# Optimization experiments

Measured on AMD Instinct MI355X. Metric: run time of the kernel, lower is better.

The kernel has to match this reference:

```python
import jax, jax.numpy as jnp
from jax import lax
import numpy as np

D_MODEL = 1024
D_STATE = 64
D_CONV = 4
EXPAND = 2
HEADDIM = 64
D_INNER = EXPAND * D_MODEL          # 2048
NHEADS = D_INNER // HEADDIM         # 32
CHUNK = 64
CONV_DIM = D_INNER + 2 * D_STATE    # 2176
D_IN_PROJ = 2 * D_INNER + 2 * D_STATE + NHEADS  # 4256
B_SZ = 4
SEQLEN = 2048
EPS = 1e-5


def _silu(x):
    return x * jax.nn.sigmoid(x)


def _segsum(x):
    # x: [..., T]; returns [..., T, T] with [i,j] = sum_{j<k<=i} x[k], -inf above diag
    T = x.shape[-1]
    xe = jnp.broadcast_to(x[..., None], x.shape + (T,))
    strict_lower = jnp.tril(jnp.ones((T, T), bool), -1)
    xe = jnp.where(strict_lower, xe, 0.0)
    s = jnp.cumsum(xe, axis=-2)
    lower = jnp.tril(jnp.ones((T, T), bool), 0)
    return jnp.where(lower, s, -jnp.inf)


def setup_inputs() -> dict:
    key = jax.random.key(0)
    ks = jax.random.split(key, 5)
    u = jax.random.normal(ks[0], (B_SZ, SEQLEN, D_MODEL), jnp.float32)
    W_in = jax.random.normal(ks[1], (D_IN_PROJ, D_MODEL), jnp.float32) * 0.02
    conv_w = jax.random.normal(ks[2], (CONV_DIM, 1, D_CONV), jnp.float32) * 0.2  # depthwise kernel
    conv_b = jnp.zeros((CONV_DIM,), jnp.float32)
    dt_bias = jax.random.uniform(ks[3], (NHEADS,), jnp.float32, -1.0, 1.0)
    A_log = jnp.log(jnp.linspace(1.0, float(NHEADS), NHEADS)).astype(jnp.float32)
    D = jnp.ones((NHEADS,), jnp.float32)
    norm_w = jnp.ones((D_INNER,), jnp.float32)
    W_out = jax.random.normal(ks[4], (D_MODEL, D_INNER), jnp.float32) * 0.02
    return dict(u=u, W_in=W_in, conv_w=conv_w, conv_b=conv_b, dt_bias=dt_bias,
                A_log=A_log, D=D, norm_w=norm_w, W_out=W_out)


def reference(u, W_in, conv_w, conv_b, dt_bias, A_log, D, norm_w, W_out):
    b, s, _ = u.shape
    A = -jnp.exp(A_log)                                   # [H]
    zxbcdt = u @ W_in.T                                   # [b,s,D_IN_PROJ]
    z = zxbcdt[..., :D_INNER]
    xBC = zxbcdt[..., D_INNER:D_INNER + CONV_DIM]
    dt = jax.nn.softplus(zxbcdt[..., D_INNER + CONV_DIM:] + dt_bias)  # [b,s,H]

    # causal depthwise conv1d (left pad d_conv-1 == torch pad-both + slice[:s])
    xc = lax.conv_general_dilated(
        xBC.transpose(0, 2, 1), conv_w, window_strides=(1,),
        padding=[(D_CONV - 1, 0)], feature_group_count=CONV_DIM,
        dimension_numbers=('NCH', 'OIH', 'NCH'))
    xBC = _silu(xc.transpose(0, 2, 1) + conv_b)           # [b,s,CONV_DIM]

    x = xBC[..., :D_INNER].reshape(b, s, NHEADS, HEADDIM)
    Bm = xBC[..., D_INNER:D_INNER + D_STATE]              # [b,s,N]
    Cm = xBC[..., D_INNER + D_STATE:]                     # [b,s,N]

    # SSD chunked scan
    nch = s // CHUNK
    xs = (x * dt[..., None]).reshape(b, nch, CHUNK, NHEADS, HEADDIM)
    Ad = (A * dt).reshape(b, nch, CHUNK, NHEADS)
    Br = Bm.reshape(b, nch, CHUNK, D_STATE)
    Cr = Cm.reshape(b, nch, CHUNK, D_STATE)
    A_ch = Ad.transpose(0, 1, 3, 2)                       # [b,c,h,l]
    A_cum = jnp.cumsum(A_ch, axis=-1)
    L = jnp.exp(_segsum(A_ch))                            # [b,c,h,l,l]
    Y_diag = jnp.einsum('bcln,bcsn,bchls,bcshp->bclhp', Cr, Br, L, xs)
    decay_states = jnp.exp(A_cum[..., -1:] - A_cum)       # [b,c,h,l]
    states = jnp.einsum('bchl,bcln,bclhp->bchpn', decay_states, Br, xs)
    init = jnp.zeros((b, 1, NHEADS, HEADDIM, D_STATE), xs.dtype)
    states = jnp.concatenate([init, states], axis=1)      # [b,c+1,h,p,n]
    total_decay = jnp.pad(A_cum[..., -1].transpose(0, 2, 1), ((0, 0), (0, 0), (1, 0)))
    decay_chunk = jnp.exp(_segsum(total_decay))           # [b,h,c+1,c+1]
    new_states = jnp.einsum('bhzc,bchpn->bzhpn', decay_chunk, states)
    states = new_states[:, :-1]                           # [b,c,h,p,n]
    state_decay_out = jnp.exp(A_cum)
    Y_off = jnp.einsum('bcln,bchpn,bchl->bclhp', Cr, states, state_decay_out)
    y = (Y_diag + Y_off).reshape(b, s, NHEADS, HEADDIM)

    y = y + x * D[:, None]
    y = y.reshape(b, s, D_INNER)
    # gated RMSNorm
    y = y * _silu(z)
    y = y * lax.rsqrt(jnp.mean(y * y, axis=-1, keepdims=True) + EPS) * norm_w
    return y @ W_out.T
```

## Files before the change

kernel.cpp:

```cpp
#include <hip/hip_runtime.h>
#include <hip/hip_bf16.h>

#define BSZ 4
#define SEQ 2048
#define DMODEL 1024
#define DINNER 2048
#define DSTATE 64
#define NH 32
#define HD 64
#define CKL 64
#define NCH 32
#define CONVD 2176
#define DPROJ 4256
#define N1 4224
#define MTOT 8192
#define YSTR 72
#define YSTR2 120
#define CVTB 6272

typedef __hip_bfloat16 bf16;
typedef __attribute__((ext_vector_type(8))) short short8;
typedef __attribute__((ext_vector_type(4))) short short4_;
typedef __attribute__((ext_vector_type(4))) float f32x4;

__device__ __forceinline__ float sigmoidf_(float x) { return 1.0f / (1.0f + __expf(-x)); }
__device__ __forceinline__ float bits2f(short s) { return __uint_as_float(((unsigned)(unsigned short)s) << 16); }
__device__ __forceinline__ short f2bits(float f) {
    bf16 h = __float2bfloat16(f);
    return *reinterpret_cast<short*>(&h);
}

__device__ __forceinline__ void gl_lds16(const bf16* g, bf16* l) {
    __builtin_amdgcn_global_load_lds((const __attribute__((address_space(1))) void*)g,
                                     (__attribute__((address_space(3))) void*)l, 16, 0, 0);
}

__device__ __forceinline__ f32x4 MF(short8 a, short8 b, f32x4 c) {
    return __builtin_amdgcn_mfma_f32_16x16x32_bf16(a, b, c, 0, 0, 0);
}

template<int N> __device__ __forceinline__ void vmw() {
    if constexpr (N == 0)      asm volatile("s_waitcnt vmcnt(0)" ::: "memory");
    else if constexpr (N == 3) asm volatile("s_waitcnt vmcnt(3)" ::: "memory");
    else if constexpr (N == 6) asm volatile("s_waitcnt vmcnt(6)" ::: "memory");
    else                       asm volatile("s_waitcnt vmcnt(15)" ::: "memory");
}

__device__ __forceinline__ void swzx(int& bx, int& by) {
    int nx = gridDim.x;
    int nwg = nx * gridDim.y;
    int Lr = blockIdx.y * nx + blockIdx.x;
    int L = (Lr & 7) * (nwg >> 3) + (Lr >> 3);
    int GSZ = nx * 8;
    int g = L / GSZ, r = L - g * GSZ;
    bx = r % nx;
    by = g * 8 + r / nx;
}

__global__ __launch_bounds__(256) void k_pre2(const float* __restrict__ u, const float* __restrict__ W_in,
                                              const float* __restrict__ dt_bias,
                                              const float* __restrict__ W_out, const float* __restrict__ nw,
                                              bf16* __restrict__ u_b, float* __restrict__ dtt,
                                              bf16* __restrict__ win_b, bf16* __restrict__ wout_b) {
    __shared__ __align__(16) float us[8 * DMODEL];
    const int tid = threadIdx.x;
    if (blockIdx.x < CVTB) {
        int g = (blockIdx.x * 256 + tid) * 4;
        if (g < N1 * DMODEL) {
            f32x4 f = *(const f32x4*)&W_in[g];
            short4_ o;
#pragma unroll
            for (int j = 0; j < 4; j++) o[j] = f2bits(f[j]);
            *(short4_*)&win_b[g] = o;
        } else if (g < N1 * DMODEL + DMODEL * DINNER) {
            int g2 = g - N1 * DMODEL;
            f32x4 f = *(const f32x4*)&W_out[g2];
            f32x4 w = *(const f32x4*)&nw[g2 & (DINNER - 1)];
            short4_ o;
#pragma unroll
            for (int j = 0; j < 4; j++) o[j] = f2bits(f[j] * w[j]);
            *(short4_*)&wout_b[g2] = o;
        }
        return;
    }
    const int t0 = (blockIdx.x - CVTB) * 8;
    const float* ur = u + (size_t)t0 * DMODEL;
    bf16* ub = u_b + (size_t)t0 * DMODEL;
#pragma unroll
    for (int i = 0; i < 8; i++) {
        int idx = (i * 256 + tid) * 4;
        f32x4 v = *(const f32x4*)&ur[idx];
        *(f32x4*)&us[idx] = v;
        short4_ o;
#pragma unroll
        for (int j = 0; j < 4; j++) o[j] = f2bits(v[j]);
        *(short4_*)&ub[idx] = o;
    }
    __syncthreads();
    const int h = tid >> 3, sub = tid & 7;
    const float* wr = W_in + (size_t)(DPROJ - NH + h) * DMODEL;
    float s[8] = {};
    for (int k = sub * 4; k < DMODEL; k += 32) {
        f32x4 w4 = *(const f32x4*)&wr[k];
#pragma unroll
        for (int rr = 0; rr < 8; rr++) {
            f32x4 u4 = *(const f32x4*)&us[rr * DMODEL + k];
            s[rr] += u4[0] * w4[0] + u4[1] * w4[1] + u4[2] * w4[2] + u4[3] * w4[3];
        }
    }
#pragma unroll
    for (int rr = 0; rr < 8; rr++) {
        s[rr] += __shfl_down(s[rr], 4, 8);
        s[rr] += __shfl_down(s[rr], 2, 8);
        s[rr] += __shfl_down(s[rr], 1, 8);
    }
    if (sub == 0) {
        float bh = dt_bias[h];
#pragma unroll
        for (int rr = 0; rr < 8; rr++) {
            float x = s[rr] + bh;
            dtt[(size_t)h * MTOT + t0 + rr] = (x > 20.f) ? x : log1pf(__expf(x));
        }
    }
}

__global__ __launch_bounds__(256) void k_dts(const float* __restrict__ dtt, const float* __restrict__ A_log,
                                             float* __restrict__ sAc, float* __restrict__ sfv,
                                             float* __restrict__ etot) {
    const int h = blockIdx.x, b = blockIdx.y;
    const int tid = threadIdx.x, w = tid >> 6, lane = tid & 63;
    const float Ah = -__expf(A_log[h]);
#pragma unroll
    for (int g = 0; g < 8; g++) {
        int c = g * 4 + w;
        int t0 = b * SEQ + c * CKL;
        float dv = dtt[(size_t)h * MTOT + t0 + lane];
        float v = Ah * dv;
#pragma unroll
        for (int d = 1; d < 64; d <<= 1) { float o = __shfl_up(v, d); if (lane >= d) v += o; }
        float tot = __shfl(v, 63);
        sAc[(size_t)h * MTOT + t0 + lane] = v;
        sfv[(size_t)h * MTOT + t0 + lane] = __expf(tot - v) * dv;
        if (lane == 63) etot[(h * BSZ + b) * NCH + c] = __expf(tot);
    }
}

#define BARWAIT()                                           \
    __builtin_amdgcn_s_barrier();                           \
    asm volatile("s_waitcnt lgkmcnt(0)" ::: "memory");      \
    __builtin_amdgcn_sched_barrier(0);                      \
    __builtin_amdgcn_s_setprio(1)
#define ENDPH()                                             \
    __builtin_amdgcn_s_setprio(0);                          \
    __builtin_amdgcn_s_barrier()

__global__ __launch_bounds__(512, 2) void k_g1(const bf16* __restrict__ Ap,
                                               const bf16* __restrict__ Wp,
                                               bf16* __restrict__ Cp) {
    __shared__ __align__(16) short sA[2][16384];
    __shared__ __align__(16) short sB[2][12288];
    const int tid = threadIdx.x;
    const int lane = tid & 63, w = tid >> 6;
    const int wm = w >> 2, wn = w & 3;
    const int lr = lane & 15, lk = lane >> 4;
    int bx, by; swzx(bx, by);
    const int m0 = by * 256, n0 = bx * 192;
    const int ld = DMODEL;

    const int r8 = tid >> 3;
    const int c8 = ((tid & 7) ^ (r8 & 7)) * 8;
    const bf16* pA = Ap + (size_t)(m0 + r8) * ld + c8;
    const bf16* pB = Wp + (size_t)(n0 + r8) * ld + c8;

    auto stA = [&](int d, int t) {
#pragma unroll
        for (int h = 0; h < 2; h++)
#pragma unroll
            for (int q = 0; q < 2; q++)
                gl_lds16(pA + (size_t)(h * 128 + q * 64) * ld + t * 64,
                         (bf16*)&sA[d][h * 8192 + q * 4096 + tid * 8]);
    };
    auto stB = [&](int d, int u, int t) {
        gl_lds16(pB + (size_t)(u * 64) * ld + t * 64,
                 (bf16*)&sB[d][u * 4096 + tid * 8]);
    };

    const int c0 = (lk ^ (lr & 7)) * 8;
    const int c1 = ((lk + 4) ^ (lr & 7)) * 8;
    const int aR = (wm * 128 + lr) * 64;
    const int bR = (wn * 48 + lr) * 64;

    f32x4 acc[8][3];
#pragma unroll
    for (int i = 0; i < 8; i++)
#pragma unroll
        for (int j = 0; j < 3; j++) acc[i][j] = (f32x4){0.f, 0.f, 0.f, 0.f};
    short8 bfr[3][2], af[2][2];

#define RDA1(D, I)                                                   \
    af[0][0] = *(const short8*)&sA[D][aR + (I) * 1024 + c0];         \
    af[0][1] = *(const short8*)&sA[D][aR + (I) * 1024 + c1];         \
    af[1][0] = *(const short8*)&sA[D][aR + (I + 1) * 1024 + c0];     \
    af[1][1] = *(const short8*)&sA[D][aR + (I + 1) * 1024 + c1]
#define RDB1(D)                                                      \
    _Pragma("unroll")                                                \
    for (int jn = 0; jn < 3; ++jn) {                                 \
        bfr[jn][0] = *(const short8*)&sB[D][bR + jn * 1024 + c0];    \
        bfr[jn][1] = *(const short8*)&sB[D][bR + jn * 1024 + c1];    \
    }
#define MM1(I)                                                       \
    _Pragma("unroll")                                                \
    for (int hh = 0; hh < 2; ++hh) {                                 \
        _Pragma("unroll")                                            \
        for (int jn = 0; jn < 3; ++jn) {                             \
            acc[I][jn]     = MF(af[0][hh], bfr[jn][hh], acc[I][jn]); \
            acc[I + 1][jn] = MF(af[1][hh], bfr[jn][hh], acc[I + 1][jn]); \
        }                                                            \
    }

    stB(0, 0, 0); stB(0, 1, 0); stB(0, 2, 0); stA(0, 0);
    stB(1, 0, 1); stB(1, 1, 1); stB(1, 2, 1);
    vmw<3>();
    __builtin_amdgcn_s_barrier();

    for (int t0 = 0; t0 < 16; t0 += 2) {
        const int t1 = t0 + 1, t2 = t0 + 2, t3 = t0 + 3;
        const bool more = (t2 < 16);
        RDB1(0); RDA1(0, 0);
        stA(1, t1);
        BARWAIT(); MM1(0); ENDPH();
        RDA1(0, 2); if (more) stB(0, 0, t2);
        BARWAIT(); MM1(2); ENDPH();
        RDA1(0, 4); if (more) stB(0, 1, t2);
        BARWAIT(); MM1(4); ENDPH();
        RDA1(0, 6); if (more) stB(0, 2, t2);
        BARWAIT(); MM1(6);
        __builtin_amdgcn_s_setprio(0);
        if (more) vmw<3>(); else vmw<0>();
        __builtin_amdgcn_s_barrier();
        RDB1(1); RDA1(1, 0);
        if (more) stA(0, t2);
        BARWAIT(); MM1(0); ENDPH();
        RDA1(1, 2); if (more) stB(1, 0, t3);
        BARWAIT(); MM1(2); ENDPH();
        RDA1(1, 4); if (more) stB(1, 1, t3);
        BARWAIT(); MM1(4); ENDPH();
        RDA1(1, 6); if (more) stB(1, 2, t3);
        BARWAIT(); MM1(6);
        __builtin_amdgcn_s_setprio(0);
        if (more) vmw<3>();
        __builtin_amdgcn_s_barrier();
    }
#undef RDA1
#undef RDB1
#undef MM1

#pragma unroll
    for (int im = 0; im < 8; im++) {
        int row = m0 + wm * 128 + im * 16 + lk * 4;
#pragma unroll
        for (int jn = 0; jn < 3; jn++) {
            int col = n0 + wn * 48 + jn * 16 + lr;
            bf16* cp = Cp + (size_t)row * N1 + col;
#pragma unroll
            for (int rr = 0; rr < 4; rr++) cp[(size_t)rr * N1] = __float2bfloat16(acc[im][jn][rr]);
        }
    }
}

__global__ __launch_bounds__(512, 2) void k_g2(const bf16* __restrict__ Ap,
                                               const bf16* __restrict__ Wp,
                                               float* __restrict__ Cp) {
    __shared__ __align__(16) short sA[3][16384];
    __shared__ __align__(16) short sB[3][8192];
    __shared__ float rsrow[256];
    const int tid = threadIdx.x;
    const int lane = tid & 63, w = tid >> 6;
    const int wm = w >> 1, wn = w & 1;
    const int lr = lane & 15, lk = lane >> 4;
    int bx, by; swzx(bx, by);
    const int m0 = by * 256, n0 = bx * 128;
    const int lda = N1, ldb = DINNER;

    const int r8 = tid >> 3;
    const int c8 = ((tid & 7) ^ (r8 & 7)) * 8;
    const bf16* pA = Ap + (size_t)(m0 + r8) * lda + c8;
    const bf16* pB = Wp + (size_t)(n0 + r8) * ldb + c8;

    auto stA = [&](int d, int t) {
#pragma unroll
        for (int h = 0; h < 2; h++)
#pragma unroll
            for (int q = 0; q < 2; q++)
                gl_lds16(pA + (size_t)(h * 128 + q * 64) * lda + t * 64,
                         (bf16*)&sA[d][h * 8192 + q * 4096 + tid * 8]);
    };
    auto stB = [&](int d, int t) {
#pragma unroll
        for (int q = 0; q < 2; q++)
            gl_lds16(pB + (size_t)(q * 64) * ldb + t * 64,
                     (bf16*)&sB[d][q * 4096 + tid * 8]);
    };

    const int c0 = (lk ^ (lr & 7)) * 8;
    const int c1 = ((lk + 4) ^ (lr & 7)) * 8;
    const int aR = (wm * 64 + lr) * 64;
    const int bR = (wn * 64 + lr) * 64;

    f32x4 acc[4][4];
#pragma unroll
    for (int i = 0; i < 4; i++)
#pragma unroll
        for (int j = 0; j < 4; j++) acc[i][j] = (f32x4){0.f, 0.f, 0.f, 0.f};
    float ssq[4] = {0.f, 0.f, 0.f, 0.f};
    short8 bfr[4][2], af[2][2];

#define RDA2(D, I)                                                   \
    af[0][0] = *(const short8*)&sA[D][aR + (I) * 1024 + c0];         \
    af[0][1] = *(const short8*)&sA[D][aR + (I) * 1024 + c1];         \
    af[1][0] = *(const short8*)&sA[D][aR + (I + 1) * 1024 + c0];     \
    af[1][1] = *(const short8*)&sA[D][aR + (I + 1) * 1024 + c1]
#define RDB2(D)                                                      \
    _Pragma("unroll")                                                \
    for (int jn = 0; jn < 4; ++jn) {                                 \
        bfr[jn][0] = *(const short8*)&sB[D][bR + jn * 1024 + c0];    \
        bfr[jn][1] = *(const short8*)&sB[D][bR + jn * 1024 + c1];    \
    }
#define MM2(I)                                                       \
    _Pragma("unroll")                                                \
    for (int hh = 0; hh < 2; ++hh) {                                 \
        _Pragma("unroll")                                            \
        for (int jn = 0; jn < 4; ++jn) {                             \
            acc[I][jn]     = MF(af[0][hh], bfr[jn][hh], acc[I][jn]); \
            acc[I + 1][jn] = MF(af[1][hh], bfr[jn][hh], acc[I + 1][jn]); \
        }                                                            \
    }
#define SSQ2(I)                                                      \
    _Pragma("unroll")                                                \
    for (int hh = 0; hh < 2; ++hh)                                   \
        _Pragma("unroll")                                            \
        for (int e = 0; e < 8; ++e) {                                \
            float v0 = bits2f(af[0][hh][e]), v1 = bits2f(af[1][hh][e]); \
            ssq[I] += v0 * v0; ssq[I + 1] += v1 * v1;                \
        }

    stB(0, 0); stA(0, 0);
    stB(1, 1); stA(1, 1);
    vmw<6>();
    __builtin_amdgcn_s_barrier();

    int rb = 0, sb = 2;
    for (int t = 0; t < 32; ++t) {
        const bool more = (t + 2 < 32);
        RDB2(rb); RDA2(rb, 0);
        if (more) stB(sb, t + 2);
        BARWAIT(); MM2(0); SSQ2(0); ENDPH();
        RDA2(rb, 2);
        if (more) stA(sb, t + 2);
        BARWAIT(); MM2(2); SSQ2(2);
        __builtin_amdgcn_s_setprio(0);
        if (more) vmw<6>(); else if (t + 1 < 32) vmw<0>();
        __builtin_amdgcn_s_barrier();
        rb = (rb == 2) ? 0 : rb + 1;
        sb = (sb == 2) ? 0 : sb + 1;
    }
#undef RDA2
#undef RDB2
#undef MM2
#undef SSQ2

#pragma unroll
    for (int im = 0; im < 4; im++) {
        float s = ssq[im];
        s += __shfl_down(s, 32);
        s += __shfl_down(s, 16);
        if (lane < 16) rsrow[wm * 64 + im * 16 + lane] = rsqrtf(s * (1.0f / DINNER) + 1e-5f);
    }
    __syncthreads();
#pragma unroll
    for (int im = 0; im < 4; im++) {
        int rl = wm * 64 + im * 16 + lk * 4;
        int row = m0 + rl;
#pragma unroll
        for (int rr = 0; rr < 4; rr++) {
            float s = rsrow[rl + rr];
#pragma unroll
            for (int jn = 0; jn < 4; jn++) {
                int col = n0 + wn * 64 + jn * 16 + lr;
                Cp[(size_t)(row + rr) * DMODEL + col] = acc[im][jn][rr] * s;
            }
        }
    }
}

__global__ __launch_bounds__(256) void k_conv(const bf16* __restrict__ zx, const float* __restrict__ cw,
                                              const float* __restrict__ cb, bf16* __restrict__ xbc) {
    const int g = blockIdx.x * 256 + threadIdx.x;
    const int c0 = (g % 544) * 4;
    const int t0 = (g / 544) * 4;
    const int s0 = t0 & (SEQ - 1);
    const short* base = (const short*)(zx + (size_t)t0 * N1 + DINNER + c0);
    f32x4 w0 = *(const f32x4*)&cw[(c0 + 0) * 4];
    f32x4 w1 = *(const f32x4*)&cw[(c0 + 1) * 4];
    f32x4 w2 = *(const f32x4*)&cw[(c0 + 2) * 4];
    f32x4 w3 = *(const f32x4*)&cw[(c0 + 3) * 4];
    f32x4 bias = *(const f32x4*)&cb[c0];
    short4_ v[7];
#pragma unroll
    for (int o = 0; o < 7; o++) {
        if (s0 + o - 3 >= 0) v[o] = *(const short4_*)(base + (long)(o - 3) * N1);
        else v[o] = (short4_){0, 0, 0, 0};
    }
#pragma unroll
    for (int j = 0; j < 4; j++) {
        f32x4 a = bias;
#pragma unroll
        for (int k = 0; k < 4; k++) {
            short4_ x = v[j + k];
            a[0] += bits2f(x[0]) * w0[k];
            a[1] += bits2f(x[1]) * w1[k];
            a[2] += bits2f(x[2]) * w2[k];
            a[3] += bits2f(x[3]) * w3[k];
        }
        short4_ o_;
#pragma unroll
        for (int jj = 0; jj < 4; jj++) o_[jj] = f2bits(a[jj] * sigmoidf_(a[jj]));
        *(short4_*)((short*)xbc + (size_t)(t0 + j) * CONVD + c0) = o_;
    }
}

__global__ __launch_bounds__(512) void k_ssd(const bf16* __restrict__ xbc, const float* __restrict__ dtt,
                                             const float* __restrict__ sAc, const float* __restrict__ sfv,
                                             const float* __restrict__ etg, const float* __restrict__ Dp,
                                             bf16* __restrict__ zx) {
    __shared__ __align__(16) short Ct[2][64 * YSTR];
    __shared__ __align__(16) short Bt[2][64 * YSTR];
    __shared__ __align__(16) short Bn[2][64 * YSTR2];
    __shared__ __align__(16) short Xt[2][32 * YSTR2];
    __shared__ __align__(16) short Sb[2][32 * YSTR];
    __shared__ __align__(16) short Gs[4 * 16 * YSTR];
    __shared__ __align__(16) float Sf[32 * 68];
    __shared__ __align__(16) float sdt2[2][64], sAc2[2][64];
    __shared__ float etl[NCH];

    const int ph = blockIdx.x, h = blockIdx.y, b = blockIdx.z;
    const int tid = threadIdx.x;
    const bool prod = tid >= 256;
    const int ct = tid & 255;
    const int lane = ct & 63, w = ct >> 6;
    const int lr = lane & 15, lk = lane >> 4;
    const float Dh = Dp[h];
    const int xcol = h * HD + ph * 32;

    const int lrow = ct >> 2, c0 = (ct & 3) * 16, px = (ct & 3) * 8;
    const int zl = 16 * w + (lane >> 2), zp = (lane & 3) * 8;

    short8 rC0, rC1, rB0, rB1, rX;
    float rdt, rsa, rsf;
    auto load_chunk = [&](int cc) {
        int rows0 = b * SEQ + cc * CKL;
        const short* rp = (const short*)(xbc + (size_t)(rows0 + lrow) * CONVD);
        rC0 = *(const short8*)&rp[DINNER + DSTATE + c0];
        rC1 = *(const short8*)&rp[DINNER + DSTATE + c0 + 8];
        rB0 = *(const short8*)&rp[DINNER + c0];
        rB1 = *(const short8*)&rp[DINNER + c0 + 8];
        rX  = *(const short8*)&rp[xcol + px];
        rdt = dtt[(size_t)h * MTOT + rows0 + (ct & 63)];
        rsa = sAc[(size_t)h * MTOT + rows0 + (ct & 63)];
        rsf = sfv[(size_t)h * MTOT + rows0 + lrow];
    };
    auto scatter = [&](int buf) {
        *(short8*)&Ct[buf][lrow * YSTR + c0] = rC0;
        *(short8*)&Ct[buf][lrow * YSTR + c0 + 8] = rC1;
        *(short8*)&Bt[buf][lrow * YSTR + c0] = rB0;
        *(short8*)&Bt[buf][lrow * YSTR + c0 + 8] = rB1;
#pragma unroll
        for (int j = 0; j < 8; j++) {
            int n0_ = c0 + j, n1_ = c0 + 8 + j, p_ = px + j;
            Bn[buf][n0_ * YSTR2 + lrow + (n0_ >> 3) * 8] = f2bits(bits2f(rB0[j]) * rsf);
            Bn[buf][n1_ * YSTR2 + lrow + (n1_ >> 3) * 8] = f2bits(bits2f(rB1[j]) * rsf);
            Xt[buf][p_ * YSTR2 + lrow + (p_ >> 3) * 8] = rX[j];
        }
        if (ct < 64) { sdt2[buf][ct] = rdt; sAc2[buf][ct] = rsa; }
    };

    for (int i = tid; i < 32 * 68; i += 512) Sf[i] = 0.f;
    for (int i = tid; i < 32 * YSTR; i += 512) Sb[0][i] = 0;
    if (tid < NCH) etl[tid] = etg[(h * BSZ + b) * NCH + tid];
    if (prod) { load_chunk(0); scatter(0); }
    __syncthreads();

    for (int c = 0; c < NCH; c++) {
        const int par = c & 1, nb = par ^ 1;
        const int rows0 = b * SEQ + c * CKL;
        if (prod) {
            if (c + 1 < NCH) { load_chunk(c + 1); scatter(nb); }
        } else {
            float etot = etl[c];
            short8 zcur = *(const short8*)((const short*)zx + (size_t)(rows0 + zl) * N1 + xcol + zp);

            short8 cf0 = *(const short8*)&Ct[par][(16 * w + lr) * YSTR + lk * 8];
            short8 cf1 = *(const short8*)&Ct[par][(16 * w + lr) * YSTR + 32 + lk * 8];
            f32x4 acc[2];
#pragma unroll
            for (int t = 0; t < 2; t++) {
                short8 s0 = *(const short8*)&Sb[par][(16 * t + lr) * YSTR + lk * 8];
                short8 s1 = *(const short8*)&Sb[par][(16 * t + lr) * YSTR + 32 + lk * 8];
                acc[t] = MF(cf0, s0, (f32x4){0.f, 0.f, 0.f, 0.f});
                acc[t] = MF(cf1, s1, acc[t]);
            }
            float sAcl[4], el[4];
#pragma unroll
            for (int rr = 0; rr < 4; rr++) { sAcl[rr] = sAc2[par][16 * w + lk * 4 + rr]; el[rr] = __expf(sAcl[rr]); }
#pragma unroll
            for (int t = 0; t < 2; t++)
#pragma unroll
                for (int rr = 0; rr < 4; rr++) acc[t][rr] *= el[rr];
            short* gw = Gs + w * 16 * YSTR;
#pragma unroll
            for (int t = 0; t < 4; t++) {
                short8 b0 = *(const short8*)&Bt[par][(16 * t + lr) * YSTR + lk * 8];
                short8 b1 = *(const short8*)&Bt[par][(16 * t + lr) * YSTR + 32 + lk * 8];
                f32x4 g = MF(cf0, b0, (f32x4){0.f, 0.f, 0.f, 0.f});
                g = MF(cf1, b1, g);
                int s = 16 * t + lr;
                float sAcs = sAc2[par][s], dts = sdt2[par][s];
#pragma unroll
                for (int rr = 0; rr < 4; rr++) {
                    int l = 16 * w + lk * 4 + rr;
                    float v = (s <= l) ? g[rr] * __expf(sAcl[rr] - sAcs) * dts : 0.f;
                    gw[(lk * 4 + rr) * YSTR + s] = f2bits(v);
                }
            }
            short8 gf0 = *(const short8*)&gw[lr * YSTR + lk * 8];
            short8 gf1 = *(const short8*)&gw[lr * YSTR + 32 + lk * 8];
#pragma unroll
            for (int t = 0; t < 2; t++) {
                int xr = 16 * t + lr;
                short8 x0 = *(const short8*)&Xt[par][xr * YSTR2 + ((xr >> 3) + lk) * 8];
                short8 x1 = *(const short8*)&Xt[par][xr * YSTR2 + 32 + ((xr >> 3) + lk) * 8];
                acc[t] = MF(gf0, x0, acc[t]);
                acc[t] = MF(gf1, x1, acc[t]);
            }
            {
                int pw = w & 1, nh2 = w >> 1;
                const int xp = 16 * pw + lr;
                short8 xt0 = *(const short8*)&Xt[par][xp * YSTR2 + ((xp >> 3) + lk) * 8];
                short8 xt1 = *(const short8*)&Xt[par][xp * YSTR2 + 32 + ((xp >> 3) + lk) * 8];
#pragma unroll
                for (int j = 0; j < 2; j++) {
                    int nt = 2 * nh2 + j;
                    int nr = 16 * nt + lr;
                    short8 b0 = *(const short8*)&Bn[par][nr * YSTR2 + ((nr >> 3) + lk) * 8];
                    short8 b1 = *(const short8*)&Bn[par][nr * YSTR2 + 32 + ((nr >> 3) + lk) * 8];
                    f32x4 sacc = MF(xt0, b0, (f32x4){0.f, 0.f, 0.f, 0.f});
                    sacc = MF(xt1, b1, sacc);
#pragma unroll
                    for (int rr = 0; rr < 4; rr++) {
                        int n = 16 * nt + lr;
                        int p = 16 * pw + lk * 4 + rr;
                        float nv = Sf[p * 68 + n] * etot + sacc[rr];
                        Sf[p * 68 + n] = nv;
                        Sb[nb][p * YSTR + n] = f2bits(nv);
                    }
                }
            }
#pragma unroll
            for (int t = 0; t < 2; t++) {
#pragma unroll
                for (int rr = 0; rr < 4; rr++) {
                    int p = 16 * t + lr;
                    int l = 16 * w + lk * 4 + rr;
                    float y = acc[t][rr] + Dh * bits2f(Xt[par][p * YSTR2 + l + (p >> 3) * 8]);
                    Ct[par][l * YSTR + p] = f2bits(y);
                }
            }
            {
                short8 y8 = *(const short8*)&Ct[par][zl * YSTR + zp];
                short* zpp = (short*)zx + (size_t)(rows0 + zl) * N1 + xcol + zp;
                short8 o;
#pragma unroll
                for (int j = 0; j < 8; j++) {
                    float z = bits2f(zcur[j]);
                    o[j] = f2bits(bits2f(y8[j]) * (z * sigmoidf_(z)));
                }
                *(short8*)zpp = o;
            }
        }
        __syncthreads();
    }
}

extern "C" void kernel_launch(void* const* d_in, const int* in_sizes, int n_in,
                              void* d_out, int out_size, void* d_ws, size_t ws_size,
                              hipStream_t stream) {
    const float* u       = (const float*)d_in[0];
    const float* W_in    = (const float*)d_in[1];
    const float* conv_w  = (const float*)d_in[2];
    const float* conv_b  = (const float*)d_in[3];
    const float* dt_bias = (const float*)d_in[4];
    const float* A_log   = (const float*)d_in[5];
    const float* Dp      = (const float*)d_in[6];
    const float* norm_w  = (const float*)d_in[7];
    const float* W_out   = (const float*)d_in[8];
    float* out = (float*)d_out;

    char* ws = (char*)d_ws;
    bf16* zx     = (bf16*)ws;  ws += (size_t)MTOT * N1 * 2;
    bf16* xbc    = (bf16*)ws;  ws += (size_t)MTOT * CONVD * 2;
    bf16* wout_b = (bf16*)ws;  ws += (size_t)DMODEL * DINNER * 2;
    float* dtt   = (float*)ws; ws += (size_t)NH * MTOT * 4;
    float* sAcw  = (float*)ws; ws += (size_t)NH * MTOT * 4;
    float* sfvw  = (float*)ws; ws += (size_t)NH * MTOT * 4;
    float* etotw = (float*)ws; ws += 64 * 1024;

    bf16* u_b   = (bf16*)d_out;
    bf16* win_b = (bf16*)((char*)d_out + (size_t)MTOT * DMODEL * 2);

    k_pre2<<<CVTB + MTOT / 8, 256, 0, stream>>>(u, W_in, dt_bias, W_out, norm_w,
                                                u_b, dtt, win_b, wout_b);
    k_dts<<<dim3(NH, BSZ), 256, 0, stream>>>(dtt, A_log, sAcw, sfvw, etotw);

    k_g1<<<dim3(N1 / 192, MTOT / 256), 512, 0, stream>>>(u_b, win_b, zx);

    k_conv<<<(MTOT / 4) * (CONVD / 4) / 256, 256, 0, stream>>>(zx, conv_w, conv_b, xbc);

    k_ssd<<<dim3(2, NH, BSZ), 512, 0, stream>>>(xbc, dtt, sAcw, sfvw, etotw, Dp, zx);

    k_g2<<<dim3(DMODEL / 128, MTOT / 256), 512, 0, stream>>>(zx, wout_b, out);
}
```

Measured before the change: 350.5 us.

## Fuse causal depthwise conv and SiLU into the SSD producer loads

Removes the standalone conv kernel and its intermediate xBC buffer. The SSD kernel's producer threads now read the raw projection output with a 4-row causal window and apply the depthwise conv, bias and SiLU in registers before scattering into shared memory. This is meant to avoid a full write and re-read of the conv activation tensor and one kernel launch. In exchange, the B/C conv is recomputed by every head block, and the producer path carries more loads and math per chunk, which could stall the consumer warps. The same pointer is now passed as both the read-only input and the written output, so correctness depends on which columns the kernel writes.

```diff
diff --git a/kernel.cpp b/kernel.cpp
--- a/kernel.cpp
+++ b/kernel.cpp
@@ -393,45 +393,10 @@
     }
 }
 
-__global__ __launch_bounds__(256) void k_conv(const bf16* __restrict__ zx, const float* __restrict__ cw,
-                                              const float* __restrict__ cb, bf16* __restrict__ xbc) {
-    const int g = blockIdx.x * 256 + threadIdx.x;
-    const int c0 = (g % 544) * 4;
-    const int t0 = (g / 544) * 4;
-    const int s0 = t0 & (SEQ - 1);
-    const short* base = (const short*)(zx + (size_t)t0 * N1 + DINNER + c0);
-    f32x4 w0 = *(const f32x4*)&cw[(c0 + 0) * 4];
-    f32x4 w1 = *(const f32x4*)&cw[(c0 + 1) * 4];
-    f32x4 w2 = *(const f32x4*)&cw[(c0 + 2) * 4];
-    f32x4 w3 = *(const f32x4*)&cw[(c0 + 3) * 4];
-    f32x4 bias = *(const f32x4*)&cb[c0];
-    short4_ v[7];
-#pragma unroll
-    for (int o = 0; o < 7; o++) {
-        if (s0 + o - 3 >= 0) v[o] = *(const short4_*)(base + (long)(o - 3) * N1);
-        else v[o] = (short4_){0, 0, 0, 0};
-    }
-#pragma unroll
-    for (int j = 0; j < 4; j++) {
-        f32x4 a = bias;
-#pragma unroll
-        for (int k = 0; k < 4; k++) {
-            short4_ x = v[j + k];
-            a[0] += bits2f(x[0]) * w0[k];
-            a[1] += bits2f(x[1]) * w1[k];
-            a[2] += bits2f(x[2]) * w2[k];
-            a[3] += bits2f(x[3]) * w3[k];
-        }
-        short4_ o_;
-#pragma unroll
-        for (int jj = 0; jj < 4; jj++) o_[jj] = f2bits(a[jj] * sigmoidf_(a[jj]));
-        *(short4_*)((short*)xbc + (size_t)(t0 + j) * CONVD + c0) = o_;
-    }
-}
-
-__global__ __launch_bounds__(512) void k_ssd(const bf16* __restrict__ xbc, const float* __restrict__ dtt,
+__global__ __launch_bounds__(512) void k_ssd(const bf16* __restrict__ xtail_src, const float* __restrict__ dtt,
                                              const float* __restrict__ sAc, const float* __restrict__ sfv,
                                              const float* __restrict__ etg, const float* __restrict__ Dp,
+                                             const float* __restrict__ cw, const float* __restrict__ cb,
                                              bf16* __restrict__ zx) {
     __shared__ __align__(16) short Ct[2][64 * YSTR];
     __shared__ __align__(16) short Bt[2][64 * YSTR];
@@ -441,6 +406,8 @@
     __shared__ __align__(16) short Gs[4 * 16 * YSTR];
     __shared__ __align__(16) float Sf[32 * 68];
     __shared__ __align__(16) float sdt2[2][64], sAc2[2][64];
+    __shared__ __align__(16) float cwB_s[512];
+    __shared__ float cbB_s[128];
     __shared__ float etl[NCH];
 
     const int ph = blockIdx.x, h = blockIdx.y, b = blockIdx.z;
@@ -455,16 +422,58 @@
     const int lrow = ct >> 2, c0 = (ct & 3) * 16, px = (ct & 3) * 8;
     const int zl = 16 * w + (lane >> 2), zp = (lane & 3) * 8;
 
+    f32x4 xw[8]; f32x4 xb0, xb1;
+    if (prod) {
+#pragma unroll
+        for (int j = 0; j < 8; j++) xw[j] = *(const f32x4*)&cw[(xcol + px + j) * 4];
+        xb0 = *(const f32x4*)&cb[xcol + px];
+        xb1 = *(const f32x4*)&cb[xcol + px + 4];
+    }
+
     short8 rC0, rC1, rB0, rB1, rX;
     float rdt, rsa, rsf;
     auto load_chunk = [&](int cc) {
         int rows0 = b * SEQ + cc * CKL;
-        const short* rp = (const short*)(xbc + (size_t)(rows0 + lrow) * CONVD);
-        rC0 = *(const short8*)&rp[DINNER + DSTATE + c0];
-        rC1 = *(const short8*)&rp[DINNER + DSTATE + c0 + 8];
-        rB0 = *(const short8*)&rp[DINNER + c0];
-        rB1 = *(const short8*)&rp[DINNER + c0 + 8];
-        rX  = *(const short8*)&rp[xcol + px];
+        int rt = rows0 + lrow;
+        int s = rt & (SEQ - 1);
+        const short* zr = (const short*)xtail_src + (size_t)rt * N1;
+        short8 tB0[4], tB1[4], tC0[4], tC1[4], tX[4];
+#pragma unroll
+        for (int k = 0; k < 4; k++) {
+            if (s + k - 3 >= 0) {
+                const short* zk = zr + (long)(k - 3) * N1;
+                tB0[k] = *(const short8*)&zk[4096 + c0];
+                tB1[k] = *(const short8*)&zk[4096 + c0 + 8];
+                tC0[k] = *(const short8*)&zk[4160 + c0];
+                tC1[k] = *(const short8*)&zk[4160 + c0 + 8];
+                tX[k]  = *(const short8*)&zk[2048 + xcol + px];
+            } else {
+                tB0[k] = tB1[k] = tC0[k] = tC1[k] = tX[k] = (short8){0, 0, 0, 0, 0, 0, 0, 0};
+            }
+        }
+#pragma unroll
+        for (int j = 0; j < 8; j++) {
+            float aB0 = cbB_s[c0 + j],      aB1 = cbB_s[c0 + 8 + j];
+            float aC0 = cbB_s[64 + c0 + j], aC1 = cbB_s[64 + c0 + 8 + j];
+            f32x4 wB0 = *(const f32x4*)&cwB_s[(c0 + j) * 4];
+            f32x4 wB1 = *(const f32x4*)&cwB_s[(c0 + 8 + j) * 4];
+            f32x4 wC0 = *(const f32x4*)&cwB_s[(64 + c0 + j) * 4];
+            f32x4 wC1 = *(const f32x4*)&cwB_s[(64 + c0 + 8 + j) * 4];
+            float aX = (j < 4) ? xb0[j] : xb1[j - 4];
+#pragma unroll
+            for (int k = 0; k < 4; k++) {
+                aB0 += bits2f(tB0[k][j]) * wB0[k];
+                aB1 += bits2f(tB1[k][j]) * wB1[k];
+                aC0 += bits2f(tC0[k][j]) * wC0[k];
+                aC1 += bits2f(tC1[k][j]) * wC1[k];
+                aX  += bits2f(tX[k][j])  * xw[j][k];
+            }
+            rB0[j] = f2bits(aB0 * sigmoidf_(aB0));
+            rB1[j] = f2bits(aB1 * sigmoidf_(aB1));
+            rC0[j] = f2bits(aC0 * sigmoidf_(aC0));
+            rC1[j] = f2bits(aC1 * sigmoidf_(aC1));
+            rX[j]  = f2bits(aX  * sigmoidf_(aX));
+        }
         rdt = dtt[(size_t)h * MTOT + rows0 + (ct & 63)];
         rsa = sAc[(size_t)h * MTOT + rows0 + (ct & 63)];
         rsf = sfv[(size_t)h * MTOT + rows0 + lrow];
@@ -487,6 +496,9 @@
     for (int i = tid; i < 32 * 68; i += 512) Sf[i] = 0.f;
     for (int i = tid; i < 32 * YSTR; i += 512) Sb[0][i] = 0;
     if (tid < NCH) etl[tid] = etg[(h * BSZ + b) * NCH + tid];
+    cwB_s[tid] = cw[2048 * 4 + tid];
+    if (tid < 128) cbB_s[tid] = cb[2048 + tid];
+    __syncthreads();
     if (prod) { load_chunk(0); scatter(0); }
     __syncthreads();
 
@@ -607,7 +619,6 @@
 
     char* ws = (char*)d_ws;
     bf16* zx     = (bf16*)ws;  ws += (size_t)MTOT * N1 * 2;
-    bf16* xbc    = (bf16*)ws;  ws += (size_t)MTOT * CONVD * 2;
     bf16* wout_b = (bf16*)ws;  ws += (size_t)DMODEL * DINNER * 2;
     float* dtt   = (float*)ws; ws += (size_t)NH * MTOT * 4;
     float* sAcw  = (float*)ws; ws += (size_t)NH * MTOT * 4;
@@ -623,9 +634,8 @@
 
     k_g1<<<dim3(N1 / 192, MTOT / 256), 512, 0, stream>>>(u_b, win_b, zx);
 
-    k_conv<<<(MTOT / 4) * (CONVD / 4) / 256, 256, 0, stream>>>(zx, conv_w, conv_b, xbc);
-
-    k_ssd<<<dim3(2, NH, BSZ), 512, 0, stream>>>(xbc, dtt, sAcw, sfvw, etotw, Dp, zx);
+    k_ssd<<<dim3(2, NH, BSZ), 512, 0, stream>>>(zx, dtt, sAcw, sfvw, etotw, Dp,
+                                                conv_w, conv_b, zx);
 
     k_g2<<<dim3(DMODEL / 128, MTOT / 256), 512, 0, stream>>>(zx, wout_b, out);
 }
```

After: 478.9 us. +36.6%, slower.
